# Optimization experiments

Hardware: AMD Instinct MI355X
Metric: run time of the kernel (lower is better)

Reference implementation:

```python
import jax, jax.numpy as jnp
import numpy as np

D_MODEL, D_HID, N_EXPERTS, TOP_K = 1024, 4096, 8, 2

def setup_inputs() -> dict:
    key = jax.random.key(0)
    ks = jax.random.split(key, 6)
    B, T = 2, 2048
    x = jax.random.normal(ks[0], (B, T, D_MODEL), dtype=jnp.float32)
    gate_w = jax.random.normal(ks[1], (N_EXPERTS, D_MODEL), dtype=jnp.float32) * (1.0 / np.sqrt(D_MODEL))
    # kaiming_uniform-ish init for expert weights
    lim1 = np.sqrt(6.0 / D_MODEL)
    lim2 = np.sqrt(6.0 / D_HID)
    w1 = jax.random.uniform(ks[2], (N_EXPERTS, D_MODEL, D_HID), dtype=jnp.float32, minval=-lim1, maxval=lim1)
    w2 = jax.random.uniform(ks[3], (N_EXPERTS, D_HID, D_MODEL), dtype=jnp.float32, minval=-lim2, maxval=lim2)
    b1 = jnp.zeros((N_EXPERTS, 1, D_HID), dtype=jnp.float32)
    b2 = jnp.zeros((N_EXPERTS, 1, D_MODEL), dtype=jnp.float32)
    return {"x": x, "gate_w": gate_w, "w1": w1, "b1": b1, "w2": w2, "b2": b2}

def reference(x, gate_w, w1, b1, w2, b2):
    B, T, D = x.shape
    E = gate_w.shape[0]
    xf = x.reshape(-1, D)                              # [N, D]
    N = xf.shape[0]
    # Router: logits -> softmax -> top-k -> renormalize
    logits = jnp.einsum('nd,ed->ne', xf, gate_w)       # [N, E]
    scores = jax.nn.softmax(logits, axis=-1)
    top_w, top_i = jax.lax.top_k(scores, TOP_K)        # [N, K]
    top_w = top_w / jnp.sum(top_w, axis=-1, keepdims=True)
    # Dense combine weights (zero for unselected experts) — same math as
    # the padded-bmm dispatch/combine: padded slots have weight 0.
    gates = jnp.zeros((N, E), xf.dtype).at[jnp.arange(N)[:, None], top_i].add(top_w)  # [N, E]
    # Grouped expert MLP (computed densely; weighted combine zeroes unrouted experts)
    h = jax.nn.gelu(jnp.einsum('nd,edh->enh', xf, w1) + b1, approximate=False)  # [E, N, H]
    expert_out = jnp.einsum('enh,ehd->end', h, w2) + b2                          # [E, N, D]
    out = jnp.einsum('end,ne->nd', expert_out, gates)                            # [N, D]
    return out.reshape(B, T, D)
```

## Files before the change

### kernel.cpp

```cpp
#include <hip/hip_runtime.h>
#include <math.h>

#define NTOK 4096
#define DM   1024
#define DH   4096
#define NE   8
#define NSLOT (NTOK*2)
#define TMAX 72

typedef unsigned short u16;
typedef __attribute__((ext_vector_type(8))) short shortx8;
typedef __attribute__((ext_vector_type(4))) float floatx4;
typedef __attribute__((ext_vector_type(4))) int   intx4;

__device__ __forceinline__ u16 f2bf(float f) {
  union { float f; unsigned u; } c; c.f = f;
  unsigned r = c.u + 0x7fffu + ((c.u >> 16) & 1u);
  return (u16)(r >> 16);
}

__device__ __forceinline__ void async_cp16(const u16* g, u16* l) {
  __builtin_amdgcn_global_load_lds(
      (const __attribute__((address_space(1))) void*)g,
      (__attribute__((address_space(3))) void*)l, 16, 0, 0);
}

__global__ void cvt_x_kernel(const float* __restrict__ x, u16* __restrict__ xb) {
  int i = (blockIdx.x * 256 + threadIdx.x) * 8;
  float4 v0 = *(const float4*)(x + i);
  float4 v1 = *(const float4*)(x + i + 4);
  u16 tmp[8] = {f2bf(v0.x), f2bf(v0.y), f2bf(v0.z), f2bf(v0.w),
                f2bf(v1.x), f2bf(v1.y), f2bf(v1.z), f2bf(v1.w)};
  *(intx4*)(xb + i) = *(intx4*)tmp;
}

template<int K, int NW>
__global__ __launch_bounds__(256) void transpose_kernel(const float* __restrict__ W,
                                                        u16* __restrict__ Wt) {
  __shared__ u16 tile[64][66];
  int e = blockIdx.z;
  int n0 = blockIdx.x * 64, k0 = blockIdx.y * 64;
  int tt = threadIdx.x;
  const float* src = W + (size_t)e * K * NW + (size_t)(k0 + (tt >> 2)) * NW + n0 + (tt & 3) * 16;
  int r = tt >> 2, c4 = (tt & 3) * 16;
  float4 v[4];
#pragma unroll
  for (int i = 0; i < 4; i++) v[i] = *(const float4*)(src + i * 4);
#pragma unroll
  for (int i = 0; i < 4; i++) {
    tile[r][c4 + 4 * i + 0] = f2bf(v[i].x);
    tile[r][c4 + 4 * i + 1] = f2bf(v[i].y);
    tile[r][c4 + 4 * i + 2] = f2bf(v[i].z);
    tile[r][c4 + 4 * i + 3] = f2bf(v[i].w);
  }
  __syncthreads();
  u16* dst = Wt + (size_t)e * NW * K + (size_t)n0 * K + k0;
#pragma unroll
  for (int p = 0; p < 2; p++) {
    int n = (tt >> 3) + p * 32;
    int kc = (tt & 7) * 8;
    u16 o[8];
#pragma unroll
    for (int i = 0; i < 8; i++) o[i] = tile[kc + i][n];
    *(intx4*)(dst + (size_t)n * K + kc) = *(intx4*)o;
  }
}

__global__ __launch_bounds__(256) void router_kernel(const float* __restrict__ x,
                                                     const float* __restrict__ gw,
                                                     int* __restrict__ eos,
                                                     float* __restrict__ wos) {
  int wave = threadIdx.x >> 6, lane = threadIdx.x & 63;
  int n = blockIdx.x * 4 + wave;
  const float* xr = x + (size_t)n * DM;
  float acc[NE];
#pragma unroll
  for (int e = 0; e < NE; e++) acc[e] = 0.f;
  for (int d = lane; d < DM; d += 64) {
    float xv = xr[d];
#pragma unroll
    for (int e = 0; e < NE; e++) acc[e] += xv * gw[e * DM + d];
  }
#pragma unroll
  for (int e = 0; e < NE; e++) {
    float v = acc[e];
#pragma unroll
    for (int off = 32; off > 0; off >>= 1) v += __shfl_xor(v, off, 64);
    acc[e] = v;
  }
  if (lane == 0) {
    int i0 = 0;
    for (int e = 1; e < NE; e++) if (acc[e] > acc[i0]) i0 = e;
    int i1 = (i0 == 0) ? 1 : 0;
    for (int e = 0; e < NE; e++) { if (e == i0) continue; if (acc[e] > acc[i1]) i1 = e; }
    float e1 = expf(acc[i1] - acc[i0]);
    float w0 = 1.f / (1.f + e1);
    eos[2 * n] = i0;  eos[2 * n + 1] = i1;
    wos[2 * n] = w0;  wos[2 * n + 1] = 1.f - w0;
  }
}

__global__ __launch_bounds__(256) void build_groups_kernel(
    const int* __restrict__ eos, const float* __restrict__ wos,
    int* __restrict__ goff, int* __restrict__ tok_of_g, float* __restrict__ w_of_g,
    int* __restrict__ tiles, int* __restrict__ ntiles) {
  __shared__ int pref[256][NE];
  __shared__ int tot[NE];
  __shared__ int ebase[NE + 1];
  int t = threadIdx.x;
  int c[NE];
#pragma unroll
  for (int e = 0; e < NE; e++) c[e] = 0;
  for (int i = 0; i < NSLOT / 256; i++) {
    int e = eos[t * (NSLOT / 256) + i];
#pragma unroll
    for (int q = 0; q < NE; q++) if (e == q) c[q]++;
  }
#pragma unroll
  for (int e = 0; e < NE; e++) pref[t][e] = c[e];
  __syncthreads();
  if (t < NE) {
    int run = 0;
    for (int i = 0; i < 256; i++) { int v = pref[i][t]; pref[i][t] = run; run += v; }
    tot[t] = run;
  }
  __syncthreads();
  if (t == 0) {
    int o = 0;
    for (int e = 0; e < NE; e++) { ebase[e] = o; o += tot[e]; }
    ebase[NE] = o;
    int nt = 0;
    for (int e = 0; e < NE; e++)
      for (int mb = 0; mb * 128 < tot[e]; mb++) tiles[nt++] = (e << 16) | mb;
    ntiles[0] = nt;
  }
  __syncthreads();
  int off[NE];
#pragma unroll
  for (int e = 0; e < NE; e++) off[e] = ebase[e] + pref[t][e];
  for (int i = 0; i < NSLOT / 256; i++) {
    int s = t * (NSLOT / 256) + i;
    int e = eos[s];
    int g = 0;
#pragma unroll
    for (int q = 0; q < NE; q++) if (e == q) { g = off[q]; off[q] = g + 1; }
    tok_of_g[g] = s >> 1;
    w_of_g[g] = wos[s];
  }
  if (t <= NE) goff[t] = ebase[t];
}

template<int K, int NOUT, int MODE, int KSPLIT>
__global__ __launch_bounds__(256) void moe_gemm(
    const u16* __restrict__ A, const u16* __restrict__ Wt, const float* __restrict__ bias,
    const int* __restrict__ goff, const int* __restrict__ tok_of_g,
    const float* __restrict__ w_of_g, const int* __restrict__ tiles,
    const int* __restrict__ ntiles,
    u16* __restrict__ Hout, float* __restrict__ Out) {
  const int KLEN = K / KSPLIT;
  int tl = blockIdx.x;
  if (tl >= ntiles[0]) return;
  int packed = tiles[tl];
  int e = packed >> 16;
  int mb = packed & 0xffff;
  int kseg = (KSPLIT > 1) ? blockIdx.z : 0;
  int gb = goff[e];
  int cntE = goff[e + 1] - gb;
  int m0 = mb * 128;
  int mvalid = cntE - m0; if (mvalid > 128) mvalid = 128;
  int gbase = gb + m0;
  int n0 = blockIdx.y * 128;
  int kbeg = kseg * KLEN;
  int tid = threadIdx.x;
  int lane = tid & 63, wave = tid >> 6;

  __shared__ __align__(16) u16 As[2][128 * 32];
  __shared__ __align__(16) u16 Bs[2][128 * 32];

  int sr = lane >> 2;
  int sc = (lane & 3) * 8;
  int scs = sc ^ (((sr >> 1) & 3) << 3);
  int ra0 = wave * 16 + sr;
  int ra1 = 64 + wave * 16 + sr;
  int ca0 = (ra0 < mvalid) ? ra0 : (mvalid - 1);
  int ca1 = (ra1 < mvalid) ? ra1 : (mvalid - 1);
  const u16 *pa0, *pa1;
  if (MODE == 0) {
    pa0 = A + (size_t)tok_of_g[gbase + ca0] * K + scs;
    pa1 = A + (size_t)tok_of_g[gbase + ca1] * K + scs;
  } else {
    pa0 = A + (size_t)(gbase + ca0) * K + scs;
    pa1 = A + (size_t)(gbase + ca1) * K + scs;
  }
  const u16* wte = Wt + (size_t)e * NOUT * K;
  const u16* pb0 = wte + (size_t)(n0 + ra0) * K + scs;
  const u16* pb1 = wte + (size_t)(n0 + ra1) * K + scs;

  int wm = wave >> 1, wn = wave & 1;
  int lr = lane & 15, lk = (lane >> 4) * 8;
  int lks = lk ^ (((lr >> 1) & 3) << 3);

  floatx4 acc[4][4];
#pragma unroll
  for (int i = 0; i < 4; i++)
#pragma unroll
    for (int j = 0; j < 4; j++) acc[i][j] = (floatx4){0.f, 0.f, 0.f, 0.f};

  auto stage = [&](int b, int k0) {
    async_cp16(pa0 + k0, &As[b][wave * 512]);
    async_cp16(pa1 + k0, &As[b][2048 + wave * 512]);
    async_cp16(pb0 + k0, &Bs[b][wave * 512]);
    async_cp16(pb1 + k0, &Bs[b][2048 + wave * 512]);
  };
  auto compute = [&](int b) {
    shortx8 af[4], bfr[4];
#pragma unroll
    for (int i = 0; i < 4; i++) {
      af[i]  = *(const shortx8*)&As[b][(wm * 64 + i * 16 + lr) * 32 + lks];
      bfr[i] = *(const shortx8*)&Bs[b][(wn * 64 + i * 16 + lr) * 32 + lks];
    }
#pragma unroll
    for (int i = 0; i < 4; i++)
#pragma unroll
      for (int j = 0; j < 4; j++)
        acc[i][j] = __builtin_amdgcn_mfma_f32_16x16x32_bf16(af[i], bfr[j], acc[i][j], 0, 0, 0);
  };

  const int NT = KLEN / 32;
  stage(0, kbeg);
  __syncthreads();
  for (int t = 0; t < NT - 2; t += 2) {
    stage(1, kbeg + (t + 1) * 32);
    compute(0);
    __syncthreads();
    stage(0, kbeg + (t + 2) * 32);
    compute(1);
    __syncthreads();
  }
  stage(1, kbeg + KLEN - 32);
  compute(0);
  __syncthreads();
  compute(1);

  const float* bp = bias + (size_t)e * NOUT + n0;
  if (MODE == 0) {
#pragma unroll
    for (int i = 0; i < 4; i++) {
      int rowb = wm * 64 + i * 16 + (lane >> 4) * 4;
#pragma unroll
      for (int r = 0; r < 4; r++) {
        int grow = rowb + r;
        if (grow < mvalid) {
          size_t base = (size_t)(gbase + grow) * NOUT + n0;
#pragma unroll
          for (int j = 0; j < 4; j++) {
            int col = wn * 64 + j * 16 + lr;
            float v = acc[i][j][r] + bp[col];
            v = 0.5f * v * (1.f + erff(v * 0.70710678118654752f));
            Hout[base + col] = f2bf(v);
          }
        }
      }
    }
  } else {
#pragma unroll
    for (int i = 0; i < 4; i++) {
      int rowb = wm * 64 + i * 16 + (lane >> 4) * 4;
#pragma unroll
      for (int r = 0; r < 4; r++) {
        int grow = rowb + r;
        if (grow < mvalid) {
          int gi = gbase + grow;
          int t = tok_of_g[gi];
          float wg = w_of_g[gi];
          float* orow = Out + (size_t)t * DM + n0;
#pragma unroll
          for (int j = 0; j < 4; j++) {
            int col = wn * 64 + j * 16 + lr;
            float bb = (kseg == 0) ? bp[col] : 0.f;
            atomicAdd(&orow[col], wg * (acc[i][j][r] + bb));
          }
        }
      }
    }
  }
}

extern "C" void kernel_launch(void* const* d_in, const int* in_sizes, int n_in,
                              void* d_out, int out_size, void* d_ws, size_t ws_size,
                              hipStream_t stream) {
  const float* x  = (const float*)d_in[0];
  const float* gw = (const float*)d_in[1];
  const float* w1 = (const float*)d_in[2];
  const float* b1 = (const float*)d_in[3];
  const float* w2 = (const float*)d_in[4];
  const float* b2 = (const float*)d_in[5];
  float* out = (float*)d_out;
  char* ws = (char*)d_ws;

  u16* xb = (u16*)(ws + 0);
  u16* wt = (u16*)(ws + 8388608);
  u16* h  = (u16*)(ws + 75497472);
  char* meta = ws + 142606336;
  int*   eos      = (int*)(meta);
  int*   tok_of_g = (int*)(meta + 32768);
  float* wos      = (float*)(meta + 65536);
  float* w_of_g   = (float*)(meta + 98304);
  int*   goff     = (int*)(meta + 131072);
  int*   tiles    = (int*)(meta + 131200);
  int*   ntiles   = (int*)(meta + 131584);

  hipMemsetAsync(out, 0, (size_t)NTOK * DM * 4, stream);

  cvt_x_kernel<<<NTOK * DM / 8 / 256, 256, 0, stream>>>(x, xb);
  transpose_kernel<DM, DH><<<dim3(DH / 64, DM / 64, NE), 256, 0, stream>>>(w1, wt);
  router_kernel<<<NTOK / 4, 256, 0, stream>>>(x, gw, eos, wos);
  build_groups_kernel<<<1, 256, 0, stream>>>(eos, wos, goff, tok_of_g, w_of_g, tiles, ntiles);
  moe_gemm<DM, DH, 0, 1><<<dim3(TMAX, DH / 128, 1), 256, 0, stream>>>(
      xb, wt, b1, goff, tok_of_g, w_of_g, tiles, ntiles, h, nullptr);
  transpose_kernel<DH, DM><<<dim3(DM / 64, DH / 64, NE), 256, 0, stream>>>(w2, wt);
  moe_gemm<DH, DM, 1, 2><<<dim3(TMAX, DM / 128, 2), 256, 0, stream>>>(
      h, wt, b2, goff, tok_of_g, w_of_g, tiles, ntiles, nullptr, out);
}
```

Baseline: 801.1 us.

## Remap MoE GEMM workgroups across XCDs and deepen async LDS prefetch pipeline

Replaces the 2D/3D grid with a flat 1D grid whose block index is remapped so that consecutive workgroups on the same XCD share the same expert tile and N-block, which should improve L2 reuse of weights and activations. The main K loop is restructured so two stages are always in flight: each iteration waits with vmcnt(4), loads fragments into registers, then issues the next async global-to-LDS copy into the just-freed buffer before running the MFMAs. This is meant to overlap global loads with compute better than the previous stage-compute-sync pattern. It relies on hand-placed waitcnt and barrier instructions, which risks ordering errors if the compiler reorders memory operations.

```diff
diff --git a/kernel.cpp b/kernel.cpp
--- a/kernel.cpp
+++ b/kernel.cpp
@@ -158,18 +158,24 @@
     const int* __restrict__ ntiles,
     u16* __restrict__ Hout, float* __restrict__ Out) {
   const int KLEN = K / KSPLIT;
-  int tl = blockIdx.x;
+  const int NB = NOUT / 128;
+  const int NWG = TMAX * NB * KSPLIT;
+  int flat = blockIdx.x;
+  int wgid = (flat & 7) * (NWG >> 3) + (flat >> 3);
+  int nb   = wgid % NB;
+  int rest = wgid / NB;
+  int tl   = rest % TMAX;
+  int kseg = rest / TMAX;
   if (tl >= ntiles[0]) return;
   int packed = tiles[tl];
   int e = packed >> 16;
   int mb = packed & 0xffff;
-  int kseg = (KSPLIT > 1) ? blockIdx.z : 0;
   int gb = goff[e];
   int cntE = goff[e + 1] - gb;
   int m0 = mb * 128;
   int mvalid = cntE - m0; if (mvalid > 128) mvalid = 128;
   int gbase = gb + m0;
-  int n0 = blockIdx.y * 128;
+  int n0 = nb * 128;
   int kbeg = kseg * KLEN;
   int tid = threadIdx.x;
   int lane = tid & 63, wave = tid >> 6;
@@ -212,13 +218,14 @@
     async_cp16(pb0 + k0, &Bs[b][wave * 512]);
     async_cp16(pb1 + k0, &Bs[b][2048 + wave * 512]);
   };
-  auto compute = [&](int b) {
-    shortx8 af[4], bfr[4];
+  auto ldfrag = [&](int b, shortx8* af, shortx8* bfr) {
 #pragma unroll
     for (int i = 0; i < 4; i++) {
       af[i]  = *(const shortx8*)&As[b][(wm * 64 + i * 16 + lr) * 32 + lks];
       bfr[i] = *(const shortx8*)&Bs[b][(wn * 64 + i * 16 + lr) * 32 + lks];
     }
+  };
+  auto domfma = [&](shortx8* af, shortx8* bfr) {
 #pragma unroll
     for (int i = 0; i < 4; i++)
 #pragma unroll
@@ -228,19 +235,33 @@
 
   const int NT = KLEN / 32;
   stage(0, kbeg);
-  __syncthreads();
-  for (int t = 0; t < NT - 2; t += 2) {
-    stage(1, kbeg + (t + 1) * 32);
-    compute(0);
-    __syncthreads();
-    stage(0, kbeg + (t + 2) * 32);
-    compute(1);
-    __syncthreads();
-  }
-  stage(1, kbeg + KLEN - 32);
-  compute(0);
-  __syncthreads();
-  compute(1);
+  stage(1, kbeg + 32);
+  for (int t = 0; t < NT - 2; ++t) {
+    int cur = t & 1;
+    asm volatile("s_waitcnt vmcnt(4)" ::: "memory");
+    __builtin_amdgcn_s_barrier();
+    shortx8 af[4], bfr[4];
+    ldfrag(cur, af, bfr);
+    asm volatile("s_waitcnt lgkmcnt(0)" ::: "memory");
+    __builtin_amdgcn_sched_barrier(0);
+    __builtin_amdgcn_s_barrier();
+    stage(cur, kbeg + (t + 2) * 32);
+    domfma(af, bfr);
+  }
+  {
+    asm volatile("s_waitcnt vmcnt(4)" ::: "memory");
+    __builtin_amdgcn_s_barrier();
+    shortx8 af[4], bfr[4];
+    ldfrag(NT & 1, af, bfr);
+    domfma(af, bfr);
+  }
+  {
+    asm volatile("s_waitcnt vmcnt(0)" ::: "memory");
+    __builtin_amdgcn_s_barrier();
+    shortx8 af[4], bfr[4];
+    ldfrag(1 - (NT & 1), af, bfr);
+    domfma(af, bfr);
+  }
 
   const float* bp = bias + (size_t)e * NOUT + n0;
   if (MODE == 0) {
@@ -316,9 +337,9 @@
   transpose_kernel<DM, DH><<<dim3(DH / 64, DM / 64, NE), 256, 0, stream>>>(w1, wt);
   router_kernel<<<NTOK / 4, 256, 0, stream>>>(x, gw, eos, wos);
   build_groups_kernel<<<1, 256, 0, stream>>>(eos, wos, goff, tok_of_g, w_of_g, tiles, ntiles);
-  moe_gemm<DM, DH, 0, 1><<<dim3(TMAX, DH / 128, 1), 256, 0, stream>>>(
+  moe_gemm<DM, DH, 0, 1><<<TMAX * (DH / 128), 256, 0, stream>>>(
       xb, wt, b1, goff, tok_of_g, w_of_g, tiles, ntiles, h, nullptr);
   transpose_kernel<DH, DM><<<dim3(DM / 64, DH / 64, NE), 256, 0, stream>>>(w2, wt);
-  moe_gemm<DH, DM, 1, 2><<<dim3(TMAX, DM / 128, 2), 256, 0, stream>>>(
+  moe_gemm<DH, DM, 1, 2><<<TMAX * (DM / 128) * 2, 256, 0, stream>>>(
       h, wt, b2, goff, tok_of_g, w_of_g, tiles, ntiles, nullptr, out);
 }
```

Result: faster. 757.5 us (-5.4%).
